# Optimization experiments

Hardware: AMD Instinct MI355X
Metric: run time of the kernel (lower is better)

Reference implementation:

```python
import jax, jax.numpy as jnp
import numpy as np
from jax import lax

B, N = 16, 8192          # batch, points per cloud
G, K = 512, 32           # num_groups, group_size
TOKEN_DIM = 384
BN_EPS = 1e-5


def setup_inputs() -> dict:
    key = jax.random.key(0)
    ks = jax.random.split(key, 8)
    w = lambda i, shape: jax.random.normal(ks[i], shape, jnp.float32) * 0.05
    return {
        "points": jax.random.normal(ks[0], (B, N, 3), jnp.float32),
        # first_conv: Conv1d(3,128,1,bias=False) -> BN(128) -> ReLU -> Conv1d(128,256,1)
        "w1": w(1, (128, 3)),
        "bn1_gamma": jnp.ones((128,), jnp.float32),
        "bn1_beta": jnp.zeros((128,), jnp.float32),
        "bn1_mean": jnp.zeros((128,), jnp.float32),
        "bn1_var": jnp.ones((128,), jnp.float32),
        "w2": w(2, (256, 128)),
        "b2": jnp.zeros((256,), jnp.float32),
        # second_conv: Conv1d(512,512,1,bias=False) -> BN(512) -> ReLU -> Conv1d(512,384,1)
        "w3": w(3, (512, 512)),
        "bn2_gamma": jnp.ones((512,), jnp.float32),
        "bn2_beta": jnp.zeros((512,), jnp.float32),
        "bn2_mean": jnp.zeros((512,), jnp.float32),
        "bn2_var": jnp.ones((512,), jnp.float32),
        "w4": w(4, (TOKEN_DIM, 512)),
        "b4": jnp.zeros((TOKEN_DIM,), jnp.float32),
    }


def _fps(xyz, num_samples):
    """Farthest point sampling. xyz: [B,N,3] -> idx [B,num_samples] (start = point 0)."""
    b, n, _ = xyz.shape
    start = jnp.zeros((b,), jnp.int32)
    init_min = jnp.full((b, n), 1e10, xyz.dtype)

    def body(carry, _):
        min_d2, last = carry
        last_pt = jnp.take_along_axis(xyz, last[:, None, None], axis=1)  # [B,1,3]
        d2 = jnp.sum((xyz - last_pt) ** 2, axis=-1)                      # [B,N]
        min_d2 = jnp.minimum(min_d2, d2)
        nxt = jnp.argmax(min_d2, axis=-1).astype(jnp.int32)
        return (min_d2, nxt), last

    _, idx = lax.scan(body, (init_min, start), None, length=num_samples)
    return idx.T  # [B,num_samples]


def _bn(x, gamma, beta, mean, var):
    # inference batchnorm over last (channel) axis
    return (x - mean) * lax.rsqrt(var + BN_EPS) * gamma + beta


def reference(points, w1, bn1_gamma, bn1_beta, bn1_mean, bn1_var, w2, b2,
              w3, bn2_gamma, bn2_beta, bn2_mean, bn2_var, w4, b4):
    xyz = points[:, :, :3]
    fidx = _fps(xyz, G)                                       # [B,G]
    centers = jnp.take_along_axis(xyz, fidx[:, :, None], 1)   # [B,G,3]

    # brute-force KNN via squared distances [B,G,N]
    pn = jnp.sum(xyz * xyz, -1)                               # [B,N]
    cn = jnp.sum(centers * centers, -1)                       # [B,G]
    d2 = cn[:, :, None] + pn[:, None, :] - 2.0 * jnp.einsum('bgc,bnc->bgn', centers, xyz)
    _, idx = lax.top_k(-d2, K)                                # [B,G,K] nearest indices

    groups = jax.vmap(lambda p, i: p[i])(points, idx)          # [B,G,K,3]
    groups = groups - centers[:, :, None, :]                   # center-relative coords

    x = groups.reshape(B * G, K, 3)                            # [M,K,3]
    # first_conv
    f = jnp.einsum('mkc,dc->mkd', x, w1)                       # [M,K,128]
    f = jax.nn.relu(_bn(f, bn1_gamma, bn1_beta, bn1_mean, bn1_var))
    f = jnp.einsum('mkd,ed->mke', f, w2) + b2                  # [M,K,256]
    g = jnp.max(f, axis=1, keepdims=True)                      # [M,1,256]
    f = jnp.concatenate([jnp.broadcast_to(g, f.shape), f], -1) # [M,K,512]
    # second_conv
    f = jnp.einsum('mke,fe->mkf', f, w3)                       # [M,K,512]
    f = jax.nn.relu(_bn(f, bn2_gamma, bn2_beta, bn2_mean, bn2_var))
    f = jnp.einsum('mkf,of->mko', f, w4) + b4                  # [M,K,384]
    tokens = jnp.max(f, axis=1).reshape(B, G, TOKEN_DIM)
    return tokens, centers
```

## Files before the change

### kernel.cpp

```cpp
#include <hip/hip_runtime.h>
#include <stdint.h>

#define PB 16
#define PN 8192
#define PG 512
#define PK 32
#define PTOK 384
#define PM (PB*PG)
#define PMK (PM*PK)
#define NWORK 240
#define NTASK (PM/4)
static constexpr float BN_EPS_C = 1e-5f;

typedef short bh8  __attribute__((ext_vector_type(8)));
typedef float f32x4 __attribute__((ext_vector_type(4)));

__device__ __forceinline__ short f2bf(float f){
  unsigned u = __float_as_uint(f);
  unsigned r = u + 0x7fffu + ((u>>16)&1u);
  return (short)(r>>16);
}
__device__ __forceinline__ float bf2f(short s){
  return __uint_as_float(((unsigned)(unsigned short)s)<<16);
}
__device__ __forceinline__ void gload16(const void* g, void* l){
  __builtin_amdgcn_global_load_lds((const __attribute__((address_space(1))) unsigned int*)g,
                                   (__attribute__((address_space(3))) unsigned int*)l,
                                   16, 0, 0);
}

__global__ __launch_bounds__(1024, 4) void mega2_kernel(
    const float* __restrict__ points, float* __restrict__ centers,
    int* __restrict__ prog, int* __restrict__ qhead,
    float* __restrict__ grp){
#pragma clang fp contract(off)
  __shared__ __align__(16) char SMEM[150528];
  const int t = threadIdx.x;
  const int lane = t & 63;

  if (blockIdx.x < PB){
    const int b = blockIdx.x;
    const float* P = points + (size_t)b*PN*3;
    float4* Lc = (float4*)SMEM;
    unsigned short* sidx = (unsigned short*)(SMEM + 131072);
    int* shist = (int*)(SMEM + 147456);
    int* spart = (int*)(SMEM + 149504);
    unsigned long long* swa = (unsigned long long*)(SMEM + 149760);
    if (t < 512) shist[t] = 0;
    if (t < 3)   swa[t] = 0ull;
    __syncthreads();
    int mycell[8];
#pragma unroll
    for (int i=0;i<8;i++){
      int j = i*1024 + t;
      float x=P[j*3+0], y=P[j*3+1], z=P[j*3+2];
      Lc[j] = make_float4(x,y,z,0.f);
      int qx=(int)fminf(fmaxf((x+4.f)*1.0f,0.f),7.f);
      int qy=(int)fminf(fmaxf((y+4.f)*1.0f,0.f),7.f);
      int qz=(int)fminf(fmaxf((z+4.f)*1.0f,0.f),7.f);
      int mc = (qx&1)|((qx&2)<<2)|((qx&4)<<4)
             | ((qy&1)<<1)|((qy&2)<<3)|((qy&4)<<5)
             | ((qz&1)<<2)|((qz&2)<<4)|((qz&4)<<6);
      mycell[i]=mc;
      atomicAdd(&shist[mc],1);
    }
    __syncthreads();
    if (t < 64){
      int acc=0;
#pragma unroll
      for (int k=0;k<8;k++){ int h=shist[t*8+k]; shist[t*8+k]=acc; acc+=h; }
      spart[t]=acc;
    }
    __syncthreads();
    if (t==0){ int acc=0; for (int k=0;k<64;k++){ int h=spart[k]; spart[k]=acc; acc+=h; } }
    __syncthreads();
    if (t < 64){
      int off=spart[t];
#pragma unroll
      for (int k=0;k<8;k++) shist[t*8+k] += off;
    }
    __syncthreads();
#pragma unroll
    for (int i=0;i<8;i++){
      int j = i*1024 + t;
      int r = atomicAdd(&shist[mycell[i]],1);
      sidx[r] = (unsigned short)j;
    }
    __syncthreads();
    float px[8],py[8],pz[8],md[8]; int lowc[8];
    float tlx=1e30f,tly=1e30f,tlz=1e30f,thx=-1e30f,thy=-1e30f,thz=-1e30f;
#pragma unroll
    for (int i=0;i<8;i++){
      int oj = sidx[t*8+i];
      float4 p4 = Lc[oj];
      float x=p4.x, y=p4.y, z=p4.z;
      px[i]=x; py[i]=y; pz[i]=z; md[i]=1e10f; lowc[i]=PN-1-oj;
      tlx=fminf(tlx,x); thx=fmaxf(thx,x);
      tly=fminf(tly,y); thy=fmaxf(thy,y);
      tlz=fminf(tlz,z); thz=fmaxf(thz,z);
    }
#pragma unroll
    for (int off=32; off; off>>=1){
      tlx=fminf(tlx,__shfl_xor(tlx,off)); thx=fmaxf(thx,__shfl_xor(thx,off));
      tly=fminf(tly,__shfl_xor(tly,off)); thy=fmaxf(thy,__shfl_xor(thy,off));
      tlz=fminf(tlz,__shfl_xor(tlz,off)); thz=fmaxf(thz,__shfl_xor(thz,off));
    }
    unsigned long long wkey = ((unsigned long long)0x7F800000u)<<32;
    float cx=P[0], cy=P[1], cz=P[2];
    if (t==0){ float* c = centers + (size_t)b*PG*3; c[0]=cx; c[1]=cy; c[2]=cz; }
    __syncthreads();
    for (int g=1; g<PG; g++){
      const int sl = g%3, ns = (g+1)%3;
      float ddx=fmaxf(fmaxf(tlx-cx, cx-thx),0.f);
      float ddy=fmaxf(fmaxf(tly-cy, cy-thy),0.f);
      float ddz=fmaxf(fmaxf(tlz-cz, cz-thz),0.f);
      float dmin2=((ddx*ddx+ddy*ddy)+ddz*ddz)*0.999999f;
      if (!(dmin2 >= __uint_as_float((unsigned)(wkey>>32)))){
        unsigned long long bk = 0ull;
#pragma unroll
        for (int i=0;i<8;i++){
          float dx=px[i]-cx, dy=py[i]-cy, dz=pz[i]-cz;
          float d2 = (dx*dx + dy*dy) + dz*dz;
          md[i] = fminf(md[i], d2);
          unsigned long long ki = ((unsigned long long)__float_as_uint(md[i])<<32)
                                | (unsigned)lowc[i];
          if (ki > bk) bk = ki;
        }
#pragma unroll
        for (int mask=32; mask; mask>>=1){
          unsigned long long o = __shfl_xor(bk, mask);
          if (o > bk) bk = o;
        }
        wkey = bk;
      }
      if (lane==0) atomicMax(&swa[sl], wkey);
      if (t==0) swa[ns] = 0ull;
      __syncthreads();
      unsigned long long w = swa[sl];
      int j = PN-1 - (int)(w & 0xFFFFFFFFu);
      float4 c4 = Lc[j];
      cx = c4.x; cy = c4.y; cz = c4.z;
      if (t==0){
        float* cc = centers + ((size_t)b*PG + g)*3;
        cc[0]=cx; cc[1]=cy; cc[2]=cz;
        if ((g & 3) == 3)
          __hip_atomic_store(prog + b, g + 1, __ATOMIC_RELEASE, __HIP_MEMORY_SCOPE_AGENT);
      }
    }
  }

  unsigned long long* ks_k = (unsigned long long*)(SMEM + 149504);
  int*   ks_idx = (int*)(SMEM + 149760);
  float* ks_c   = (float*)(SMEM + 150272);
  int*   s_task = (int*)(SMEM + 150320);

  for(;;){
    if (t == 0){
      int id = atomicAdd(qhead, 1);
      s_task[0] = id;
      if (id < NTASK){
        int bb = id & (PB-1), qq = id >> 4;
        int need = qq*4 + 4;
        while (__hip_atomic_load(prog + bb, __ATOMIC_ACQUIRE, __HIP_MEMORY_SCOPE_AGENT) < need)
          __builtin_amdgcn_s_sleep(10);
      }
    }
    __syncthreads();
    const int id = s_task[0];
    if (id >= NTASK) break;
    const int b = id & (PB-1), q = id >> 4;
    const int m0 = b*PG + q*4;
    const float* P = points + (size_t)b*PN*3;
    const int sub = t >> 8, tt = t & 255;

    if (tt == 0){
      const float* cp = centers + (size_t)(m0 + sub)*3;
      ks_c[sub*3+0] = __hip_atomic_load(cp+0, __ATOMIC_ACQUIRE, __HIP_MEMORY_SCOPE_AGENT);
      ks_c[sub*3+1] = __hip_atomic_load(cp+1, __ATOMIC_ACQUIRE, __HIP_MEMORY_SCOPE_AGENT);
      ks_c[sub*3+2] = __hip_atomic_load(cp+2, __ATOMIC_ACQUIRE, __HIP_MEMORY_SCOPE_AGENT);
    }
    __syncthreads();
    {
      const float cx=ks_c[sub*3+0], cy=ks_c[sub*3+1], cz=ks_c[sub*3+2];
      const float cn = (cx*cx + cy*cy) + cz*cz;
      unsigned key[PK];
#pragma unroll
      for (int i=0;i<PK;i++){
        int j = i*256 + tt;
        float x=P[j*3+0], y=P[j*3+1], z=P[j*3+2];
        float pn = (x*x + y*y) + z*z;
        float e  = (cx*x + cy*y) + cz*z;
        float d2 = (cn + pn) - 2.0f*e;
        unsigned u = __float_as_uint(d2);
        u ^= (u & 0x80000000u) ? 0xFFFFFFFFu : 0x80000000u;
        key[i] = u;
      }
      unsigned lmin = key[0]; int li = 0;
#pragma unroll
      for (int i=1;i<PK;i++) if (key[i] < lmin){ lmin = key[i]; li = i; }
      unsigned long long lkey = ((unsigned long long)lmin << 32)
                              | (unsigned)(li*256 + tt);
      const int widx = tt >> 6;
      for (int it=0; it<PK; it++){
        unsigned long long v = lkey;
#pragma unroll
        for (int off=32; off; off>>=1){
          unsigned long long o = __shfl_down(v, off);
          if (o < v) v = o;
        }
        if (lane==0) ks_k[sub*8 + (it&1)*4 + widx] = v;
        __syncthreads();
        unsigned long long w = ks_k[sub*8 + (it&1)*4 + 0];
#pragma unroll
        for (int qq=1;qq<4;qq++){
          unsigned long long o = ks_k[sub*8 + (it&1)*4 + qq];
          if (o < w) w = o;
        }
        int wj = (int)(w & 0xFFFFFFFFull);
        if (tt==0) ks_idx[sub*32 + it] = wj;
        if ((wj & 255) == tt){
          int slot = wj >> 8;
#pragma unroll
          for (int i=0;i<PK;i++) if (i == slot) key[i] = 0xFFFFFFFFu;
          lmin = key[0]; li = 0;
#pragma unroll
          for (int i=1;i<PK;i++) if (key[i] < lmin){ lmin = key[i]; li = i; }
          lkey = ((unsigned long long)lmin << 32) | (unsigned)(li*256 + tt);
        }
      }
      __syncthreads();
      if (tt < PK*3){
        int k = tt/3, c = tt - k*3;
        int j = ks_idx[sub*32 + k];
        grp[((size_t)(m0 + sub)*PK + k)*3 + c] = P[j*3+c] - ks_c[sub*3+c];
      }
    }
  }
}

__global__ __launch_bounds__(512, 2) void mlp_kernel(const float* __restrict__ grp,
                                                     const float* __restrict__ w1,
                                                     const float* __restrict__ sc1,
                                                     const float* __restrict__ sh1,
                                                     const short* __restrict__ w2b,
                                                     const float* __restrict__ b2,
                                                     const short* __restrict__ w3ab,
                                                     const short* __restrict__ w3bb,
                                                     const float* __restrict__ sc2,
                                                     const float* __restrict__ sh2,
                                                     const short* __restrict__ w4b,
                                                     const float* __restrict__ b4,
                                                     float* __restrict__ tokens){
  __shared__ __align__(16) short s_f1f3[16384];
  __shared__ __align__(16) short s_f2[32768];
  __shared__ __align__(16) short s_g[1024];
  __shared__ __align__(16) short s_bst[24576];
  const int t = threadIdx.x;
  const int lane = t & 63, wid = t >> 6;
  const int mh = wid >> 1, nq = wid & 1;
  const int B0 = blockIdx.x * 128;
  const int G0 = blockIdx.x * 4;
  const int srow = lane >> 2;
  const int scol = (lane & 3) * 8;
  const int frow = lane & 15;
  const int fk   = (lane >> 4) * 8;
  const int rb   = (lane >> 4) * 4;
  const int cb   = lane & 15;

  {
    int r = t & 127, dg = t >> 7;
    float x0 = grp[(size_t)(B0+r)*3 + 0];
    float x1 = grp[(size_t)(B0+r)*3 + 1];
    float x2 = grp[(size_t)(B0+r)*3 + 2];
#pragma unroll
    for (int dd=0; dd<32; dd++){
      int d = dg*32 + dd;
      float a = x0*w1[d*3+0] + x1*w1[d*3+1] + x2*w1[d*3+2];
      float y = a*sc1[d] + sh1[d];
      s_f1f3[dg*4096 + r*32 + dd] = f2bf(fmaxf(y, 0.f));
    }
  }
  __syncthreads();

  {
    f32x4 accB[2][8] = {};
    for (int k0=0; k0<128; k0+=64){
      for (int cc=wid; cc<32; cc+=8){
        int sub = cc & 1, rc = cc >> 1;
        int r = rc*16 + srow;
        gload16(w2b + (size_t)r*128 + k0 + sub*32 + scol, &s_bst[sub*8192 + rc*512]);
      }
      __syncthreads();
#pragma unroll
      for (int sub=0; sub<2; sub++){
        int kc = (k0 + sub*32) >> 5;
        bh8 af[2], bf[8];
#pragma unroll
        for (int i=0;i<2;i++)
          af[i] = *(const bh8*)&s_f1f3[kc*4096 + (mh*32 + i*16 + frow)*32 + fk];
#pragma unroll
        for (int j=0;j<8;j++)
          bf[j] = *(const bh8*)&s_bst[sub*8192 + (nq*128 + j*16 + frow)*32 + fk];
#pragma unroll
        for (int i=0;i<2;i++)
#pragma unroll
          for (int j=0;j<8;j++)
            accB[i][j] = __builtin_amdgcn_mfma_f32_16x16x32_bf16(af[i], bf[j], accB[i][j], 0,0,0);
      }
      __syncthreads();
    }
#pragma unroll
    for (int i=0;i<2;i++)
#pragma unroll
      for (int j=0;j<8;j++){
        int col = nq*128 + j*16 + cb;
#pragma unroll
        for (int r=0;r<4;r++){
          int row = mh*32 + i*16 + rb + r;
          s_f2[(col>>5)*4096 + row*32 + (col&31)] = f2bf(accB[i][j][r] + b2[col]);
        }
      }
  }
  __syncthreads();

  {
#pragma unroll
    for (int task=0; task<2; task++){
      int g = (t>>8) + task*2;
      int col = t & 255;
      int kc = col >> 5, c5 = col & 31;
      float mx = -3.4e38f;
#pragma unroll
      for (int kk=0; kk<PK; kk++)
        mx = fmaxf(mx, bf2f(s_f2[kc*4096 + (g*32 + kk)*32 + c5]));
      s_g[g*256 + col] = f2bf(mx);
    }
  }
  __syncthreads();

  f32x4 acc4[2][12] = {};
  for (int nc=0; nc<4; nc++){
    f32x4 acc3[2][4] = {};
    for (int k0=0; k0<512; k0+=64){
      const short* w3s = (k0 < 256) ? w3ab : w3bb;
      int kk0 = (k0 < 256) ? k0 : (k0 - 256);
      for (int cc=wid; cc<16; cc+=8){
        int sub = cc & 1, rc = cc >> 1;
        int r = nc*128 + rc*16 + srow;
        gload16(w3s + (size_t)r*256 + kk0 + sub*32 + scol, &s_bst[sub*4096 + rc*512]);
      }
      __syncthreads();
#pragma unroll
      for (int sub=0; sub<2; sub++){
        int k = k0 + sub*32;
        bh8 af[2], bf[4];
        if (k < 256){
#pragma unroll
          for (int i=0;i<2;i++)
            af[i] = *(const bh8*)&s_g[mh*256 + k + fk];
        } else {
          int kc = (k - 256) >> 5;
#pragma unroll
          for (int i=0;i<2;i++)
            af[i] = *(const bh8*)&s_f2[kc*4096 + (mh*32 + i*16 + frow)*32 + fk];
        }
#pragma unroll
        for (int j=0;j<4;j++)
          bf[j] = *(const bh8*)&s_bst[sub*4096 + (nq*64 + j*16 + frow)*32 + fk];
#pragma unroll
        for (int i=0;i<2;i++)
#pragma unroll
          for (int j=0;j<4;j++)
            acc3[i][j] = __builtin_amdgcn_mfma_f32_16x16x32_bf16(af[i], bf[j], acc3[i][j], 0,0,0);
      }
      __syncthreads();
    }
#pragma unroll
    for (int i=0;i<2;i++)
#pragma unroll
      for (int j=0;j<4;j++){
        int cl = nq*64 + j*16 + cb;
        int f  = nc*128 + cl;
        float s = sc2[f], h = sh2[f];
#pragma unroll
        for (int r=0;r<4;r++){
          int row = mh*32 + i*16 + rb + r;
          float v = acc3[i][j][r]*s + h;
          s_f1f3[(cl>>5)*4096 + row*32 + (cl&31)] = f2bf(fmaxf(v, 0.f));
        }
      }
    __syncthreads();
    for (int kk0=0; kk0<128; kk0+=64){
      for (int cc=wid; cc<48; cc+=8){
        int sub = cc & 1, rc = cc >> 1;
        int r = rc*16 + srow;
        gload16(w4b + (size_t)r*512 + nc*128 + kk0 + sub*32 + scol, &s_bst[sub*12288 + rc*512]);
      }
      __syncthreads();
#pragma unroll
      for (int sub=0; sub<2; sub++){
        int kc = (kk0 + sub*32) >> 5;
        bh8 af[2], bf[12];
#pragma unroll
        for (int i=0;i<2;i++)
          af[i] = *(const bh8*)&s_f1f3[kc*4096 + (mh*32 + i*16 + frow)*32 + fk];
#pragma unroll
        for (int j=0;j<12;j++)
          bf[j] = *(const bh8*)&s_bst[sub*12288 + (nq*192 + j*16 + frow)*32 + fk];
#pragma unroll
        for (int i=0;i<2;i++)
#pragma unroll
          for (int j=0;j<12;j++)
            acc4[i][j] = __builtin_amdgcn_mfma_f32_16x16x32_bf16(af[i], bf[j], acc4[i][j], 0,0,0);
      }
      __syncthreads();
    }
  }

#pragma unroll
  for (int j=0;j<12;j++){
    int col = nq*192 + j*16 + cb;
    float mx = -3.4e38f;
#pragma unroll
    for (int i=0;i<2;i++)
#pragma unroll
      for (int r=0;r<4;r++)
        mx = fmaxf(mx, acc4[i][j][r]);
    mx = fmaxf(mx, __shfl_xor(mx, 16));
    mx = fmaxf(mx, __shfl_xor(mx, 32));
    if (lane < 16)
      tokens[(size_t)(G0 + mh)*PTOK + col] = mx + b4[col];
  }
}

__global__ __launch_bounds__(256) void prep_kernel(const float* __restrict__ w2,
    const float* __restrict__ w3, const float* __restrict__ w4,
    const float* __restrict__ g1, const float* __restrict__ be1,
    const float* __restrict__ mu1, const float* __restrict__ va1,
    const float* __restrict__ g2, const float* __restrict__ be2,
    const float* __restrict__ mu2, const float* __restrict__ va2,
    short* __restrict__ w2b, short* __restrict__ w3ab, short* __restrict__ w3bb,
    short* __restrict__ w4b, float* __restrict__ sc1, float* __restrict__ sh1,
    float* __restrict__ sc2, float* __restrict__ sh2,
    int* __restrict__ prog, int* __restrict__ qhead){
  int i = blockIdx.x*256 + threadIdx.x;
  if (i < 256*128) w2b[i] = f2bf(w2[i]);
  if (i < 512*512){
    int f = i >> 9, e = i & 511;
    short v = f2bf(w3[i]);
    if (e < 256) w3ab[f*256 + e] = v; else w3bb[f*256 + (e-256)] = v;
  }
  if (i < 384*512) w4b[i] = f2bf(w4[i]);
  if (i < 128){ float s = g1[i]*rsqrtf(va1[i] + BN_EPS_C); sc1[i]=s; sh1[i]=be1[i]-mu1[i]*s; }
  if (i < 512){ float s = g2[i]*rsqrtf(va2[i] + BN_EPS_C); sc2[i]=s; sh2[i]=be2[i]-mu2[i]*s; }
  if (i < PB) prog[i] = 0;
  if (i == PB) qhead[0] = 0;
}

extern "C" void kernel_launch(void* const* d_in, const int* in_sizes, int n_in,
                              void* d_out, int out_size, void* d_ws, size_t ws_size,
                              hipStream_t stream){
  const float* points = (const float*)d_in[0];
  const float* w1  = (const float*)d_in[1];
  const float* g1  = (const float*)d_in[2];
  const float* be1 = (const float*)d_in[3];
  const float* mu1 = (const float*)d_in[4];
  const float* va1 = (const float*)d_in[5];
  const float* w2  = (const float*)d_in[6];
  const float* b2  = (const float*)d_in[7];
  const float* w3  = (const float*)d_in[8];
  const float* g2  = (const float*)d_in[9];
  const float* be2 = (const float*)d_in[10];
  const float* mu2 = (const float*)d_in[11];
  const float* va2 = (const float*)d_in[12];
  const float* w4  = (const float*)d_in[13];
  const float* b4  = (const float*)d_in[14];
  float* tokens  = (float*)d_out;
  float* centers = (float*)d_out + (size_t)PM*PTOK;

  char* ws = (char*)d_ws;
  float* grp  = (float*)(ws + 0);
  short* w2b  = (short*)(ws + 3145728ull);
  short* w3ab = (short*)(ws + 3211264ull);
  short* w3bb = (short*)(ws + 3473408ull);
  short* w4b  = (short*)(ws + 3735552ull);
  float* sc1  = (float*)(ws + 4128768ull);
  float* sh1  = (float*)(ws + 4129280ull);
  float* sc2  = (float*)(ws + 4129792ull);
  float* sh2  = (float*)(ws + 4131840ull);
  int*   prog = (int*)(ws + 4133888ull);
  int*   qhead= (int*)(ws + 4133952ull);

  prep_kernel<<<1024, 256, 0, stream>>>(w2, w3, w4, g1, be1, mu1, va1, g2, be2, mu2, va2,
                                        w2b, w3ab, w3bb, w4b, sc1, sh1, sc2, sh2,
                                        prog, qhead);
  mega2_kernel<<<PB + NWORK, 1024, 0, stream>>>(points, centers, prog, qhead, grp);
  mlp_kernel<<<PMK/128, 512, 0, stream>>>(grp, w1, sc1, sh1, w2b, b2,
                                          w3ab, w3bb, sc2, sh2, w4b, b4, tokens);
}
```

Before: 1.043 ms.

## Load MLP weight fragments directly from global memory instead of LDS staging

Removes the LDS staging buffer for w2/w3/w4 and the global_load_lds copies, so each wave reads its bf16 weight fragments straight from global (L2-cached) memory into registers. This drops many __syncthreads barriers and frees 48KB of LDS, which may allow more blocks per CU. It also loads the broadcast group-max fragment once and reuses it for both row tiles. The cost is redundant global reads of the same weights by every wave, plus exposed global-load latency on the MFMA path.

```diff
diff --git a/kernel.cpp b/kernel.cpp
--- a/kernel.cpp
+++ b/kernel.cpp
@@ -22,11 +22,6 @@
 }
 __device__ __forceinline__ float bf2f(short s){
   return __uint_as_float(((unsigned)(unsigned short)s)<<16);
-}
-__device__ __forceinline__ void gload16(const void* g, void* l){
-  __builtin_amdgcn_global_load_lds((const __attribute__((address_space(1))) unsigned int*)g,
-                                   (__attribute__((address_space(3))) unsigned int*)l,
-                                   16, 0, 0);
 }
 
 __global__ __launch_bounds__(1024, 4) void mega2_kernel(
@@ -254,14 +249,11 @@
   __shared__ __align__(16) short s_f1f3[16384];
   __shared__ __align__(16) short s_f2[32768];
   __shared__ __align__(16) short s_g[1024];
-  __shared__ __align__(16) short s_bst[24576];
   const int t = threadIdx.x;
   const int lane = t & 63, wid = t >> 6;
   const int mh = wid >> 1, nq = wid & 1;
   const int B0 = blockIdx.x * 128;
   const int G0 = blockIdx.x * 4;
-  const int srow = lane >> 2;
-  const int scol = (lane & 3) * 8;
   const int frow = lane & 15;
   const int fk   = (lane >> 4) * 8;
   const int rb   = (lane >> 4) * 4;
@@ -284,30 +276,20 @@
 
   {
     f32x4 accB[2][8] = {};
-    for (int k0=0; k0<128; k0+=64){
-      for (int cc=wid; cc<32; cc+=8){
-        int sub = cc & 1, rc = cc >> 1;
-        int r = rc*16 + srow;
-        gload16(w2b + (size_t)r*128 + k0 + sub*32 + scol, &s_bst[sub*8192 + rc*512]);
-      }
-      __syncthreads();
-#pragma unroll
-      for (int sub=0; sub<2; sub++){
-        int kc = (k0 + sub*32) >> 5;
-        bh8 af[2], bf[8];
-#pragma unroll
-        for (int i=0;i<2;i++)
-          af[i] = *(const bh8*)&s_f1f3[kc*4096 + (mh*32 + i*16 + frow)*32 + fk];
+#pragma unroll
+    for (int kc=0; kc<4; kc++){
+      bh8 af[2], bf[8];
+#pragma unroll
+      for (int i=0;i<2;i++)
+        af[i] = *(const bh8*)&s_f1f3[kc*4096 + (mh*32 + i*16 + frow)*32 + fk];
+#pragma unroll
+      for (int j=0;j<8;j++)
+        bf[j] = *(const bh8*)&w2b[(size_t)(nq*128 + j*16 + frow)*128 + kc*32 + fk];
+#pragma unroll
+      for (int i=0;i<2;i++)
 #pragma unroll
         for (int j=0;j<8;j++)
-          bf[j] = *(const bh8*)&s_bst[sub*8192 + (nq*128 + j*16 + frow)*32 + fk];
-#pragma unroll
-        for (int i=0;i<2;i++)
-#pragma unroll
-          for (int j=0;j<8;j++)
-            accB[i][j] = __builtin_amdgcn_mfma_f32_16x16x32_bf16(af[i], bf[j], accB[i][j], 0,0,0);
-      }
-      __syncthreads();
+          accB[i][j] = __builtin_amdgcn_mfma_f32_16x16x32_bf16(af[i], bf[j], accB[i][j], 0,0,0);
     }
 #pragma unroll
     for (int i=0;i<2;i++)
@@ -341,40 +323,31 @@
   f32x4 acc4[2][12] = {};
   for (int nc=0; nc<4; nc++){
     f32x4 acc3[2][4] = {};
-    for (int k0=0; k0<512; k0+=64){
-      const short* w3s = (k0 < 256) ? w3ab : w3bb;
-      int kk0 = (k0 < 256) ? k0 : (k0 - 256);
-      for (int cc=wid; cc<16; cc+=8){
-        int sub = cc & 1, rc = cc >> 1;
-        int r = nc*128 + rc*16 + srow;
-        gload16(w3s + (size_t)r*256 + kk0 + sub*32 + scol, &s_bst[sub*4096 + rc*512]);
-      }
-      __syncthreads();
-#pragma unroll
-      for (int sub=0; sub<2; sub++){
-        int k = k0 + sub*32;
-        bh8 af[2], bf[4];
-        if (k < 256){
-#pragma unroll
-          for (int i=0;i<2;i++)
-            af[i] = *(const bh8*)&s_g[mh*256 + k + fk];
-        } else {
-          int kc = (k - 256) >> 5;
-#pragma unroll
-          for (int i=0;i<2;i++)
-            af[i] = *(const bh8*)&s_f2[kc*4096 + (mh*32 + i*16 + frow)*32 + fk];
-        }
+#pragma unroll 4
+    for (int kk=0; kk<16; kk++){
+      int k = kk*32;
+      const short* w3s = (k < 256) ? w3ab : w3bb;
+      int kb = (k < 256) ? k : (k - 256);
+      bh8 af[2], bf[4];
+      if (k < 256){
+        bh8 gv = *(const bh8*)&s_g[mh*256 + k + fk];
+        af[0] = gv; af[1] = gv;
+      } else {
+        int kc = (k - 256) >> 5;
+#pragma unroll
+        for (int i=0;i<2;i++)
+          af[i] = *(const bh8*)&s_f2[kc*4096 + (mh*32 + i*16 + frow)*32 + fk];
+      }
+#pragma unroll
+      for (int j=0;j<4;j++)
+        bf[j] = *(const bh8*)&w3s[(size_t)(nc*128 + nq*64 + j*16 + frow)*256 + kb + fk];
+#pragma unroll
+      for (int i=0;i<2;i++)
 #pragma unroll
         for (int j=0;j<4;j++)
-          bf[j] = *(const bh8*)&s_bst[sub*4096 + (nq*64 + j*16 + frow)*32 + fk];
-#pragma unroll
-        for (int i=0;i<2;i++)
-#pragma unroll
-          for (int j=0;j<4;j++)
-            acc3[i][j] = __builtin_amdgcn_mfma_f32_16x16x32_bf16(af[i], bf[j], acc3[i][j], 0,0,0);
-      }
-      __syncthreads();
-    }
+          acc3[i][j] = __builtin_amdgcn_mfma_f32_16x16x32_bf16(af[i], bf[j], acc3[i][j], 0,0,0);
+    }
+    __syncthreads();
 #pragma unroll
     for (int i=0;i<2;i++)
 #pragma unroll
@@ -390,30 +363,27 @@
         }
       }
     __syncthreads();
-    for (int kk0=0; kk0<128; kk0+=64){
-      for (int cc=wid; cc<48; cc+=8){
-        int sub = cc & 1, rc = cc >> 1;
-        int r = rc*16 + srow;
-        gload16(w4b + (size_t)r*512 + nc*128 + kk0 + sub*32 + scol, &s_bst[sub*12288 + rc*512]);
-      }
-      __syncthreads();
-#pragma unroll
-      for (int sub=0; sub<2; sub++){
-        int kc = (kk0 + sub*32) >> 5;
-        bh8 af[2], bf[12];
+#pragma unroll
+    for (int kk=0; kk<4; kk++){
+      int kcol = nc*128 + kk*32;
+      bh8 af[2];
+#pragma unroll
+      for (int i=0;i<2;i++)
+        af[i] = *(const bh8*)&s_f1f3[kk*4096 + (mh*32 + i*16 + frow)*32 + fk];
+#pragma unroll
+      for (int half=0; half<2; half++){
+        bh8 bf[6];
+#pragma unroll
+        for (int j=0;j<6;j++){
+          int jj = half*6 + j;
+          bf[j] = *(const bh8*)&w4b[(size_t)(nq*192 + jj*16 + frow)*512 + kcol + fk];
+        }
 #pragma unroll
         for (int i=0;i<2;i++)
-          af[i] = *(const bh8*)&s_f1f3[kc*4096 + (mh*32 + i*16 + frow)*32 + fk];
-#pragma unroll
-        for (int j=0;j<12;j++)
-          bf[j] = *(const bh8*)&s_bst[sub*12288 + (nq*192 + j*16 + frow)*32 + fk];
-#pragma unroll
-        for (int i=0;i<2;i++)
-#pragma unroll
-          for (int j=0;j<12;j++)
-            acc4[i][j] = __builtin_amdgcn_mfma_f32_16x16x32_bf16(af[i], bf[j], acc4[i][j], 0,0,0);
-      }
-      __syncthreads();
+#pragma unroll
+          for (int j=0;j<6;j++)
+            acc4[i][half*6+j] = __builtin_amdgcn_mfma_f32_16x16x32_bf16(af[i], bf[j], acc4[i][half*6+j], 0,0,0);
+      }
     }
   }
 
```

New measurement: 1.617 ms. 1.55x slower.
